# Optimization experiments

Hardware: AMD Instinct MI355X
Metric: run time of the kernel (lower is better)

Reference implementation:

```python
import jax, jax.numpy as jnp
import numpy as np

HIDDEN = 2048
N_HEADS = 32
N_KV_HEADS = 8
HEAD_DIM = HIDDEN // N_HEADS  # 64
N_GROUPS = N_HEADS // N_KV_HEADS  # 4
B, S = 1, 2048
NEG_INF = -1e9


def setup_inputs() -> dict:
    key = jax.random.key(0)
    k1, k2, k3, k4, k5 = jax.random.split(key, 5)
    hidden_states = jax.random.normal(k1, (B, S, HIDDEN), dtype=jnp.float32)
    # additive causal mask [B,1,S,S]
    causal = jnp.triu(jnp.full((S, S), NEG_INF, dtype=jnp.float32), k=1)
    attention_mask = jnp.broadcast_to(causal[None, None], (B, 1, S, S))
    position_ids = jnp.broadcast_to(jnp.arange(S, dtype=jnp.int32)[None], (B, S))
    scale = 0.02
    Wq = jax.random.normal(k2, (HIDDEN, N_HEADS * HEAD_DIM), dtype=jnp.float32) * scale
    Wk = jax.random.normal(k3, (HIDDEN, N_KV_HEADS * HEAD_DIM), dtype=jnp.float32) * scale
    Wv = jax.random.normal(k4, (HIDDEN, N_KV_HEADS * HEAD_DIM), dtype=jnp.float32) * scale
    Wo = jax.random.normal(k5, (HIDDEN, HIDDEN), dtype=jnp.float32) * scale
    return {"hidden_states": hidden_states, "attention_mask": attention_mask,
            "position_ids": position_ids, "Wq": Wq, "Wk": Wk, "Wv": Wv, "Wo": Wo}


def _rotate_half(x):
    x1, x2 = jnp.split(x, 2, axis=-1)
    return jnp.concatenate([-x2, x1], axis=-1)


def _rope_tables(kv_seq_len):
    inv_freq = 1.0 / (10000.0 ** (jnp.arange(0, HEAD_DIM, 2, dtype=jnp.float32) / HEAD_DIM))
    pos = jnp.arange(kv_seq_len, dtype=jnp.float32)
    freqs = pos[:, None] * inv_freq[None, :]          # [S, HD/2]
    emb = jnp.concatenate([freqs, freqs], axis=-1)    # [S, HD]
    return jnp.sin(emb), jnp.cos(emb)


def reference(hidden_states, attention_mask, position_ids, Wq, Wk, Wv, Wo):
    b, s, _ = hidden_states.shape
    q = (hidden_states @ Wq).reshape(b, s, N_HEADS, HEAD_DIM).transpose(0, 2, 1, 3)
    k = (hidden_states @ Wk).reshape(b, s, N_KV_HEADS, HEAD_DIM).transpose(0, 2, 1, 3)
    v = (hidden_states @ Wv).reshape(b, s, N_KV_HEADS, HEAD_DIM).transpose(0, 2, 1, 3)

    sin, cos = _rope_tables(s)
    cos_p = cos[position_ids][:, None]  # [B,1,S,HD]
    sin_p = sin[position_ids][:, None]
    q = q * cos_p + _rotate_half(q) * sin_p
    k = k * cos_p + _rotate_half(k) * sin_p

    # GQA: repeat_interleave kv heads along head axis
    k = jnp.repeat(k, N_GROUPS, axis=1)  # [B,H,S,HD]
    v = jnp.repeat(v, N_GROUPS, axis=1)

    q = q / jnp.sqrt(jnp.asarray(HEAD_DIM, q.dtype))
    scores = jnp.einsum('bhqd,bhkd->bhqk', q, k) + attention_mask
    attn = jax.nn.softmax(scores, axis=-1)
    out = jnp.einsum('bhqk,bhkd->bhqd', attn, v)
    out = out.transpose(0, 2, 1, 3).reshape(b, s, HIDDEN)
    return out @ Wo
```

## Files before the change

kernel.cpp:

```cpp
#include <hip/hip_runtime.h>
#include <hip/hip_bf16.h>

#define S_LEN 2048
#define HID 2048

typedef __attribute__((ext_vector_type(8))) short s16x8;
typedef __attribute__((ext_vector_type(4))) float f32x4;
typedef unsigned short u16;

__device__ __forceinline__ u16 f2bf(float f) {
  __hip_bfloat16 h = __float2bfloat16(f);
  return __builtin_bit_cast(u16, h);
}
__device__ __forceinline__ float bf2f(u16 u) {
  __hip_bfloat16 h = __builtin_bit_cast(__hip_bfloat16, u);
  return __bfloat162float(h);
}

#define GLD16(dst, src)                                                        \
  __builtin_amdgcn_global_load_lds(                                            \
      (__attribute__((address_space(1))) void*)(src),                          \
      (__attribute__((address_space(3))) void*)(dst), 16, 0, 0)

__global__ __launch_bounds__(256) void f2b_kernel(const float* __restrict__ in,
                                                  u16* __restrict__ outp, int n4) {
  int idx = blockIdx.x * 256 + threadIdx.x;
  if (idx >= n4) return;
  float4 v = *((const float4*)in + idx);
  ushort4 o;
  o.x = f2bf(v.x); o.y = f2bf(v.y); o.z = f2bf(v.z); o.w = f2bf(v.w);
  *((ushort4*)outp + idx) = o;
}

__global__ __launch_bounds__(256) void wtrans_kernel(const float* __restrict__ in,
                                                     u16* __restrict__ outp, int K, int N) {
  __shared__ u16 tile[32][33];
  int n0 = blockIdx.x * 32, k0 = blockIdx.y * 32;
  int tx = threadIdx.x & 31, ty = threadIdx.x >> 5;
#pragma unroll
  for (int r = 0; r < 4; ++r) {
    int row = ty + r * 8;
    tile[row][tx] = f2bf(in[(size_t)(k0 + row) * N + n0 + tx]);
  }
  __syncthreads();
#pragma unroll
  for (int r = 0; r < 4; ++r) {
    int row = ty + r * 8;
    outp[(size_t)(n0 + row) * K + k0 + tx] = tile[tx][row];
  }
}

__global__ __launch_bounds__(256) void wtransQKV_kernel(const float* __restrict__ Wq,
                                                        const float* __restrict__ Wk,
                                                        const float* __restrict__ Wv,
                                                        u16* __restrict__ outp) {
  __shared__ u16 tile[32][33];
  int n0g = blockIdx.x * 32, k0 = blockIdx.y * 32;
  const float* src;
  int n0, N;
  if (n0g < 2048)      { src = Wq; n0 = n0g;        N = 2048; }
  else if (n0g < 2560) { src = Wk; n0 = n0g - 2048; N = 512; }
  else                 { src = Wv; n0 = n0g - 2560; N = 512; }
  int tx = threadIdx.x & 31, ty = threadIdx.x >> 5;
#pragma unroll
  for (int r = 0; r < 4; ++r) {
    int row = ty + r * 8;
    tile[row][tx] = f2bf(src[(size_t)(k0 + row) * N + n0 + tx]);
  }
  __syncthreads();
#pragma unroll
  for (int r = 0; r < 4; ++r) {
    int row = ty + r * 8;
    outp[(size_t)(n0g + row) * HID + k0 + tx] = tile[tx][row];
  }
}

template <bool OUT_F32>
__global__ __launch_bounds__(256) void gemm_bt_kernel(const u16* __restrict__ A,
                                                      const u16* __restrict__ Bt,
                                                      void* __restrict__ C,
                                                      int N, int K, int sx) {
  __shared__ u16 lA[2][64 * 64];
  __shared__ u16 lB[2][128 * 64];
  int tid = threadIdx.x;
  int lane = tid & 63, w = tid >> 6;
  int lo = lane & 15, hi = lane >> 4;
  int wr = w >> 1, wc = w & 1;
  int blk = blockIdx.x;
  int j = blk & 7, q = blk >> 3;
  int bx = j * sx + (q % sx);
  int by = q / sx;
  int brow = by * 64, bcol = bx * 128;
  int l8 = lane >> 3;
  int cs = ((lane & 7) ^ l8) * 8;

  f32x4 z = {0.f, 0.f, 0.f, 0.f};
  f32x4 acc[2][4];
#pragma unroll
  for (int m = 0; m < 2; ++m)
#pragma unroll
    for (int n = 0; n < 4; ++n) acc[m][n] = z;

  const u16* Abase = A + (size_t)brow * K;
  const u16* Bbase = Bt + (size_t)bcol * K;

#define GSTAGE(buf, k0)                                                                   \
  {                                                                                       \
    _Pragma("unroll") for (int r2 = 0; r2 < 2; ++r2) {                                    \
      int c = r2 * 4 + w;                                                                 \
      GLD16(&lA[buf][c * 512], Abase + (size_t)(c * 8 + l8) * K + (k0) + cs);             \
    }                                                                                     \
    _Pragma("unroll") for (int r2 = 0; r2 < 4; ++r2) {                                    \
      int c = r2 * 4 + w;                                                                 \
      GLD16(&lB[buf][c * 512], Bbase + (size_t)(c * 8 + l8) * K + (k0) + cs);             \
    }                                                                                     \
  }

  int nsteps = K >> 6;
  int cur = 0;
  GSTAGE(0, 0);
  __syncthreads();

  for (int t = 0; t < nsteps; ++t) {
    if (t + 1 < nsteps) GSTAGE(cur ^ 1, (t + 1) * 64);

    s16x8 af[2][2], bfr[4][2];
#pragma unroll
    for (int m = 0; m < 2; ++m)
#pragma unroll
      for (int kk = 0; kk < 2; ++kk)
        af[m][kk] = *(const s16x8*)(&lA[cur][0] + (size_t)(wr * 32 + m * 16 + lo) * 64 +
                                    ((kk * 4 + hi) ^ (lo & 7)) * 8);
#pragma unroll
    for (int n = 0; n < 4; ++n)
#pragma unroll
      for (int kk = 0; kk < 2; ++kk)
        bfr[n][kk] = *(const s16x8*)(&lB[cur][0] + (size_t)(wc * 64 + n * 16 + lo) * 64 +
                                     ((kk * 4 + hi) ^ (lo & 7)) * 8);
    __builtin_amdgcn_s_setprio(1);
#pragma unroll
    for (int kk = 0; kk < 2; ++kk)
#pragma unroll
      for (int m = 0; m < 2; ++m)
#pragma unroll
        for (int n = 0; n < 4; ++n)
          acc[m][n] = __builtin_amdgcn_mfma_f32_16x16x32_bf16(af[m][kk], bfr[n][kk], acc[m][n], 0, 0, 0);
    __builtin_amdgcn_s_setprio(0);
    __syncthreads();
    cur ^= 1;
  }
#undef GSTAGE

#pragma unroll
  for (int m = 0; m < 2; ++m)
#pragma unroll
    for (int n = 0; n < 4; ++n)
#pragma unroll
      for (int r = 0; r < 4; ++r) {
        int row = brow + wr * 32 + m * 16 + hi * 4 + r;
        int col = bcol + wc * 64 + n * 16 + lo;
        if (OUT_F32)
          ((float*)C)[(size_t)row * N + col] = acc[m][n][r];
        else
          ((u16*)C)[(size_t)row * N + col] = f2bf(acc[m][n][r]);
      }
}

__global__ __launch_bounds__(256) void rope_kernel(const u16* __restrict__ in,
                                                   u16* __restrict__ Qout,
                                                   u16* __restrict__ Kout,
                                                   const int* __restrict__ pos_ids) {
  int idx = blockIdx.x * 256 + threadIdx.x;
  int i = idx & 31;
  int t2 = idx >> 5;
  int hh, s;
  const u16* base;
  u16* outp;
  float scale;
  if (t2 < S_LEN * 32) {
    hh = t2 & 31; s = t2 >> 5;
    base = in + (size_t)s * 3072 + hh * 64;
    outp = Qout + ((size_t)hh * S_LEN + s) * 64;
    scale = 0.125f * 1.44269504f;
  } else {
    int t3 = t2 - S_LEN * 32;
    hh = t3 & 7; s = t3 >> 3;
    base = in + (size_t)s * 3072 + 2048 + hh * 64;
    outp = Kout + ((size_t)hh * S_LEN + s) * 64;
    scale = 1.0f;
  }
  float pos = (float)pos_ids[s];
  float inv = exp2f(-(float)i * (13.2877124f / 32.f));
  float ang = pos * inv;
  float c = cosf(ang), sn = sinf(ang);
  float q1 = bf2f(base[i]);
  float q2 = bf2f(base[i + 32]);
  outp[i] = f2bf((q1 * c - q2 * sn) * scale);
  outp[i + 32] = f2bf((q2 * c + q1 * sn) * scale);
}

__global__ __launch_bounds__(256) void vtrans_kernel(const u16* __restrict__ in,
                                                     u16* __restrict__ outp,
                                                     int in_stride, int in_off) {
  __shared__ u16 tile[32][33];
  int s0 = blockIdx.x * 32, d0 = blockIdx.y * 32;
  int tx = threadIdx.x & 31, ty = threadIdx.x >> 5;
#pragma unroll
  for (int r = 0; r < 4; ++r) {
    int row = ty + r * 8;
    tile[row][tx] = in[(size_t)(s0 + row) * in_stride + in_off + d0 + tx];
  }
  __syncthreads();
#pragma unroll
  for (int r = 0; r < 4; ++r) {
    int row = ty + r * 8;
    outp[(size_t)(d0 + row) * S_LEN + s0 + tx] = tile[tx][row];
  }
}

__global__ __launch_bounds__(512) void attn_kernel(const u16* __restrict__ Qr,
                                                   const u16* __restrict__ Kr,
                                                   const u16* __restrict__ Vt,
                                                   u16* __restrict__ AO) {
  __shared__ u16 lK[2][2][64 * 64];
  __shared__ u16 lV[2][2][64 * 64];
  __shared__ u16 lP[8][16 * 64];
  int g = blockIdx.x & 7;
  int qt = 63 - (blockIdx.x >> 3);
  int q0 = qt * 32;
  int tid = threadIdx.x, lane = tid & 63, w = tid >> 6;
  int lo = lane & 15, hi = lane >> 4;
  int w2 = w >> 2;
  int h = g * 4 + (w & 3);
  int tmax = (q0 + 31) >> 7;
  int l8 = lane >> 3;
  int cs = ((lane & 7) ^ l8) * 8;

  const u16* Kbase = Kr + (size_t)g * S_LEN * 64;
  const u16* Vbase = Vt + (size_t)g * 64 * S_LEN;
  u16* Pw = &lP[w][0];

#define STAGE_KV(buf, t)                                                                  \
  {                                                                                       \
    _Pragma("unroll") for (int hs = 0; hs < 2; ++hs) {                                    \
      GLD16(&lK[buf][hs][w * 512],                                                        \
            Kbase + ((size_t)((t) * 128 + hs * 64 + w * 8 + l8)) * 64 + cs);              \
      GLD16(&lV[buf][hs][w * 512],                                                        \
            Vbase + ((size_t)(w * 8 + l8)) * S_LEN + (t) * 128 + hs * 64 + cs);           \
    }                                                                                     \
  }

  f32x4 z = {0.f, 0.f, 0.f, 0.f};

  s16x8 aq[2];
  {
    const u16* qp = Qr + ((size_t)h * S_LEN + q0 + w2 * 16) * 64;
#pragma unroll
    for (int kk = 0; kk < 2; ++kk)
      aq[kk] = *(const s16x8*)(qp + (size_t)lo * 64 + kk * 32 + hi * 8);
  }

  f32x4 oacc[4];
#pragma unroll
  for (int n = 0; n < 4; ++n) oacc[n] = z;
  float mrun[4], ps[4];
#pragma unroll
  for (int r = 0; r < 4; ++r) { mrun[r] = -1e30f; ps[r] = 0.f; }

  int cur = 0;
  STAGE_KV(0, 0);
  __syncthreads();

  for (int t = 0; t <= tmax; ++t) {
    if (t < tmax) STAGE_KV(cur ^ 1, t + 1);

    f32x4 sacc[2][4];
#pragma unroll
    for (int hs = 0; hs < 2; ++hs)
#pragma unroll
      for (int n = 0; n < 4; ++n) sacc[hs][n] = z;
    __builtin_amdgcn_s_setprio(1);
#pragma unroll
    for (int hs = 0; hs < 2; ++hs)
#pragma unroll
      for (int kk = 0; kk < 2; ++kk)
#pragma unroll
        for (int n = 0; n < 4; ++n) {
          s16x8 bk = *(const s16x8*)(&lK[cur][hs][0] + (size_t)(n * 16 + lo) * 64 +
                                     ((kk * 4 + hi) ^ (lo & 7)) * 8);
          sacc[hs][n] = __builtin_amdgcn_mfma_f32_16x16x32_bf16(aq[kk], bk, sacc[hs][n], 0, 0, 0);
        }
    __builtin_amdgcn_s_setprio(0);

    if (t == tmax) {
#pragma unroll
      for (int hs = 0; hs < 2; ++hs)
#pragma unroll
        for (int n = 0; n < 4; ++n)
#pragma unroll
          for (int r = 0; r < 4; ++r) {
            int qg = q0 + w2 * 16 + hi * 4 + r;
            int kg = t * 128 + hs * 64 + n * 16 + lo;
            if (kg > qg) sacc[hs][n][r] = -1e30f;
          }
    }

    float tm[4];
#pragma unroll
    for (int r = 0; r < 4; ++r) {
      float a = fmaxf(fmaxf(sacc[0][0][r], sacc[0][1][r]), fmaxf(sacc[0][2][r], sacc[0][3][r]));
      float b = fmaxf(fmaxf(sacc[1][0][r], sacc[1][1][r]), fmaxf(sacc[1][2][r], sacc[1][3][r]));
      tm[r] = fmaxf(a, b);
    }
#pragma unroll
    for (int off = 1; off < 16; off <<= 1)
#pragma unroll
      for (int r = 0; r < 4; ++r) tm[r] = fmaxf(tm[r], __shfl_xor(tm[r], off, 64));

    float growth = -1e30f;
#pragma unroll
    for (int r = 0; r < 4; ++r) growth = fmaxf(growth, tm[r] - mrun[r]);
    if (__any(growth > 12.f)) {
#pragma unroll
      for (int r = 0; r < 4; ++r) {
        float nm = fmaxf(mrun[r], tm[r]);
        float scl = __builtin_amdgcn_exp2f(mrun[r] - nm);
        mrun[r] = nm;
        ps[r] *= scl;
#pragma unroll
        for (int n = 0; n < 4; ++n) oacc[n][r] *= scl;
      }
    }
#pragma unroll
    for (int hs = 0; hs < 2; ++hs)
#pragma unroll
      for (int n = 0; n < 4; ++n)
#pragma unroll
        for (int r = 0; r < 4; ++r)
          sacc[hs][n][r] = __builtin_amdgcn_exp2f(sacc[hs][n][r] - mrun[r]);
#pragma unroll
    for (int r = 0; r < 4; ++r)
      ps[r] += sacc[0][0][r] + sacc[0][1][r] + sacc[0][2][r] + sacc[0][3][r] +
               sacc[1][0][r] + sacc[1][1][r] + sacc[1][2][r] + sacc[1][3][r];

#pragma unroll
    for (int hs = 0; hs < 2; ++hs) {
#pragma unroll
      for (int r = 0; r < 4; ++r) {
        int row = hi * 4 + r;
#pragma unroll
        for (int n = 0; n < 4; ++n) {
          int col = (n * 16 + lo) ^ ((row & 7) * 8);
          Pw[row * 64 + col] = f2bf(sacc[hs][n][r]);
        }
      }
      __builtin_amdgcn_s_setprio(1);
#pragma unroll
      for (int kk = 0; kk < 2; ++kk) {
        s16x8 ap = *(const s16x8*)(Pw + (size_t)lo * 64 + ((kk * 4 + hi) ^ (lo & 7)) * 8);
#pragma unroll
        for (int n = 0; n < 4; ++n) {
          s16x8 bv = *(const s16x8*)(&lV[cur][hs][0] + (size_t)(n * 16 + lo) * 64 +
                                     ((kk * 4 + hi) ^ (lo & 7)) * 8);
          oacc[n] = __builtin_amdgcn_mfma_f32_16x16x32_bf16(ap, bv, oacc[n], 0, 0, 0);
        }
      }
      __builtin_amdgcn_s_setprio(0);
    }

    __syncthreads();
    cur ^= 1;
  }

#pragma unroll
  for (int off = 1; off < 16; off <<= 1)
#pragma unroll
    for (int r = 0; r < 4; ++r) ps[r] += __shfl_xor(ps[r], off, 64);

#pragma unroll
  for (int n = 0; n < 4; ++n)
#pragma unroll
    for (int r = 0; r < 4; ++r) {
      int q = q0 + w2 * 16 + hi * 4 + r;
      int d = n * 16 + lo;
      AO[(size_t)q * HID + h * 64 + d] = f2bf(oacc[n][r] / ps[r]);
    }
#undef STAGE_KV
}

extern "C" void kernel_launch(void* const* d_in, const int* in_sizes, int n_in,
                              void* d_out, int out_size, void* d_ws, size_t ws_size,
                              hipStream_t stream) {
  const float* X  = (const float*)d_in[0];
  const int*   pos = (const int*)d_in[2];
  const float* Wq = (const float*)d_in[3];
  const float* Wk = (const float*)d_in[4];
  const float* Wv = (const float*)d_in[5];
  const float* Wo = (const float*)d_in[6];
  float* out = (float*)d_out;

  u16* Xb    = (u16*)d_ws;
  u16* WQKVt = Xb + (size_t)HID * HID;
  u16* Kr    = WQKVt;
  u16* Vt    = WQKVt + (size_t)8 * S_LEN * 64;
  u16* Wot   = WQKVt + (size_t)16 * S_LEN * 64;
  u16* QKVp  = WQKVt + (size_t)3072 * HID;
  u16* Qr    = Xb;
  u16* AO    = QKVp;

  f2b_kernel<<<(S_LEN * HID / 4 + 255) / 256, 256, 0, stream>>>(X, Xb, S_LEN * HID / 4);
  wtransQKV_kernel<<<dim3(3072 / 32, HID / 32), 256, 0, stream>>>(Wq, Wk, Wv, WQKVt);

  gemm_bt_kernel<false><<<dim3(768), 256, 0, stream>>>(Xb, WQKVt, QKVp, 3072, HID, 3);

  wtrans_kernel<<<dim3(HID / 32, HID / 32), 256, 0, stream>>>(Wo, Wot, HID, HID);

  rope_kernel<<<(S_LEN * 40 * 32) / 256, 256, 0, stream>>>(QKVp, Qr, Kr, pos);
  vtrans_kernel<<<dim3(S_LEN / 32, 512 / 32), 256, 0, stream>>>(QKVp, Vt, 3072, 2560);

  attn_kernel<<<dim3(512), 512, 0, stream>>>(Qr, Kr, Vt, AO);

  gemm_bt_kernel<true><<<dim3(512), 256, 0, stream>>>(AO, Wot, out, HID, HID, 2);
}
```

Before: 240.3 us.

## Enlarge GEMM tiles to 128x128 with 8 waves and vectorize weight transposes

The bf16 GEMM block tile grows from 64x128 with 4 waves to 128x128 with 8 waves, so each block reuses the staged B tile across twice as many rows and the grid shrinks by half. The weight transpose kernels switch to 64x64 tiles that read with float4 loads and write 16-byte vectors, aiming to cut memory transactions in the preprocessing stage. Trade-offs are more LDS per block, fewer blocks for the 256-CU device (the output GEMM drops to 256 blocks), and possible LDS bank conflicts on the column reads of the transpose tile.

```diff
diff --git a/kernel.cpp b/kernel.cpp
--- a/kernel.cpp
+++ b/kernel.cpp
@@ -32,74 +32,79 @@
   *((ushort4*)outp + idx) = o;
 }
 
-__global__ __launch_bounds__(256) void wtrans_kernel(const float* __restrict__ in,
-                                                     u16* __restrict__ outp, int K, int N) {
-  __shared__ u16 tile[32][33];
-  int n0 = blockIdx.x * 32, k0 = blockIdx.y * 32;
-  int tx = threadIdx.x & 31, ty = threadIdx.x >> 5;
-#pragma unroll
-  for (int r = 0; r < 4; ++r) {
-    int row = ty + r * 8;
-    tile[row][tx] = f2bf(in[(size_t)(k0 + row) * N + n0 + tx]);
+__device__ __forceinline__ void wtrans64_body(const float* __restrict__ src, int N,
+                                              u16* __restrict__ outp, int orow0,
+                                              int n0, int k0, int tid) {
+  __shared__ u16 tile[64][66];
+  int tr = tid >> 4;
+  int tc4 = (tid & 15) * 4;
+#pragma unroll
+  for (int rr = 0; rr < 4; ++rr) {
+    int r = tr + rr * 16;
+    float4 v = *(const float4*)&src[(size_t)(k0 + r) * N + n0 + tc4];
+    tile[r][tc4 + 0] = f2bf(v.x);
+    tile[r][tc4 + 1] = f2bf(v.y);
+    tile[r][tc4 + 2] = f2bf(v.z);
+    tile[r][tc4 + 3] = f2bf(v.w);
   }
   __syncthreads();
-#pragma unroll
-  for (int r = 0; r < 4; ++r) {
-    int row = ty + r * 8;
-    outp[(size_t)(n0 + row) * K + k0 + tx] = tile[tx][row];
-  }
+  int n = tid >> 2;
+  int k16 = (tid & 3) * 16;
+  s16x8 a, b;
+#pragma unroll
+  for (int j = 0; j < 8; ++j) {
+    a[j] = (short)tile[k16 + j][n];
+    b[j] = (short)tile[k16 + 8 + j][n];
+  }
+  u16* dst = outp + (size_t)(orow0 + n) * HID + k0 + k16;
+  *(s16x8*)dst = a;
+  *(s16x8*)(dst + 8) = b;
 }
 
 __global__ __launch_bounds__(256) void wtransQKV_kernel(const float* __restrict__ Wq,
                                                         const float* __restrict__ Wk,
                                                         const float* __restrict__ Wv,
                                                         u16* __restrict__ outp) {
-  __shared__ u16 tile[32][33];
-  int n0g = blockIdx.x * 32, k0 = blockIdx.y * 32;
+  int n0g = blockIdx.x * 64, k0 = blockIdx.y * 64;
   const float* src;
   int n0, N;
   if (n0g < 2048)      { src = Wq; n0 = n0g;        N = 2048; }
   else if (n0g < 2560) { src = Wk; n0 = n0g - 2048; N = 512; }
   else                 { src = Wv; n0 = n0g - 2560; N = 512; }
-  int tx = threadIdx.x & 31, ty = threadIdx.x >> 5;
-#pragma unroll
-  for (int r = 0; r < 4; ++r) {
-    int row = ty + r * 8;
-    tile[row][tx] = f2bf(src[(size_t)(k0 + row) * N + n0 + tx]);
-  }
-  __syncthreads();
-#pragma unroll
-  for (int r = 0; r < 4; ++r) {
-    int row = ty + r * 8;
-    outp[(size_t)(n0g + row) * HID + k0 + tx] = tile[tx][row];
-  }
+  wtrans64_body(src, N, outp, n0g, n0, k0, threadIdx.x);
+}
+
+__global__ __launch_bounds__(256) void wtransO_kernel(const float* __restrict__ Wo,
+                                                      u16* __restrict__ outp) {
+  int n0 = blockIdx.x * 64, k0 = blockIdx.y * 64;
+  wtrans64_body(Wo, 2048, outp, n0, n0, k0, threadIdx.x);
 }
 
 template <bool OUT_F32>
-__global__ __launch_bounds__(256) void gemm_bt_kernel(const u16* __restrict__ A,
-                                                      const u16* __restrict__ Bt,
-                                                      void* __restrict__ C,
-                                                      int N, int K, int sx) {
-  __shared__ u16 lA[2][64 * 64];
+__global__ __launch_bounds__(512, 4) void gemm_bt_kernel(const u16* __restrict__ A,
+                                                         const u16* __restrict__ Bt,
+                                                         void* __restrict__ C,
+                                                         int N, int K, int sx) {
+  __shared__ u16 lA[2][128 * 64];
   __shared__ u16 lB[2][128 * 64];
   int tid = threadIdx.x;
   int lane = tid & 63, w = tid >> 6;
   int lo = lane & 15, hi = lane >> 4;
-  int wr = w >> 1, wc = w & 1;
+  int wr = w >> 2, wc = w & 3;
   int blk = blockIdx.x;
   int j = blk & 7, q = blk >> 3;
   int bx = j * sx + (q % sx);
   int by = q / sx;
-  int brow = by * 64, bcol = bx * 128;
+  int brow = by * 128, bcol = bx * 128;
   int l8 = lane >> 3;
   int cs = ((lane & 7) ^ l8) * 8;
 
   f32x4 z = {0.f, 0.f, 0.f, 0.f};
-  f32x4 acc[2][4];
-#pragma unroll
-  for (int m = 0; m < 2; ++m)
-#pragma unroll
-    for (int n = 0; n < 4; ++n) acc[m][n] = z;
+  f32x4 acc[4][2];
+#pragma unroll
+  for (int m = 0; m < 4; ++m)
+#pragma unroll
+    for (int n = 0; n < 2; ++n) acc[m][n] = z;
 
   const u16* Abase = A + (size_t)brow * K;
   const u16* Bbase = Bt + (size_t)bcol * K;
@@ -107,11 +112,8 @@
 #define GSTAGE(buf, k0)                                                                   \
   {                                                                                       \
     _Pragma("unroll") for (int r2 = 0; r2 < 2; ++r2) {                                    \
-      int c = r2 * 4 + w;                                                                 \
+      int c = r2 * 8 + w;                                                                 \
       GLD16(&lA[buf][c * 512], Abase + (size_t)(c * 8 + l8) * K + (k0) + cs);             \
-    }                                                                                     \
-    _Pragma("unroll") for (int r2 = 0; r2 < 4; ++r2) {                                    \
-      int c = r2 * 4 + w;                                                                 \
       GLD16(&lB[buf][c * 512], Bbase + (size_t)(c * 8 + l8) * K + (k0) + cs);             \
     }                                                                                     \
   }
@@ -124,26 +126,26 @@
   for (int t = 0; t < nsteps; ++t) {
     if (t + 1 < nsteps) GSTAGE(cur ^ 1, (t + 1) * 64);
 
-    s16x8 af[2][2], bfr[4][2];
-#pragma unroll
-    for (int m = 0; m < 2; ++m)
+    s16x8 af[4][2], bfr[2][2];
+#pragma unroll
+    for (int m = 0; m < 4; ++m)
 #pragma unroll
       for (int kk = 0; kk < 2; ++kk)
-        af[m][kk] = *(const s16x8*)(&lA[cur][0] + (size_t)(wr * 32 + m * 16 + lo) * 64 +
+        af[m][kk] = *(const s16x8*)(&lA[cur][0] + (size_t)(wr * 64 + m * 16 + lo) * 64 +
                                     ((kk * 4 + hi) ^ (lo & 7)) * 8);
 #pragma unroll
-    for (int n = 0; n < 4; ++n)
+    for (int n = 0; n < 2; ++n)
 #pragma unroll
       for (int kk = 0; kk < 2; ++kk)
-        bfr[n][kk] = *(const s16x8*)(&lB[cur][0] + (size_t)(wc * 64 + n * 16 + lo) * 64 +
+        bfr[n][kk] = *(const s16x8*)(&lB[cur][0] + (size_t)(wc * 32 + n * 16 + lo) * 64 +
                                      ((kk * 4 + hi) ^ (lo & 7)) * 8);
     __builtin_amdgcn_s_setprio(1);
 #pragma unroll
     for (int kk = 0; kk < 2; ++kk)
 #pragma unroll
-      for (int m = 0; m < 2; ++m)
-#pragma unroll
-        for (int n = 0; n < 4; ++n)
+      for (int m = 0; m < 4; ++m)
+#pragma unroll
+        for (int n = 0; n < 2; ++n)
           acc[m][n] = __builtin_amdgcn_mfma_f32_16x16x32_bf16(af[m][kk], bfr[n][kk], acc[m][n], 0, 0, 0);
     __builtin_amdgcn_s_setprio(0);
     __syncthreads();
@@ -152,13 +154,13 @@
 #undef GSTAGE
 
 #pragma unroll
-  for (int m = 0; m < 2; ++m)
-#pragma unroll
-    for (int n = 0; n < 4; ++n)
+  for (int m = 0; m < 4; ++m)
+#pragma unroll
+    for (int n = 0; n < 2; ++n)
 #pragma unroll
       for (int r = 0; r < 4; ++r) {
-        int row = brow + wr * 32 + m * 16 + hi * 4 + r;
-        int col = bcol + wc * 64 + n * 16 + lo;
+        int row = brow + wr * 64 + m * 16 + hi * 4 + r;
+        int col = bcol + wc * 32 + n * 16 + lo;
         if (OUT_F32)
           ((float*)C)[(size_t)row * N + col] = acc[m][n][r];
         else
@@ -409,16 +411,16 @@
   u16* AO    = QKVp;
 
   f2b_kernel<<<(S_LEN * HID / 4 + 255) / 256, 256, 0, stream>>>(X, Xb, S_LEN * HID / 4);
-  wtransQKV_kernel<<<dim3(3072 / 32, HID / 32), 256, 0, stream>>>(Wq, Wk, Wv, WQKVt);
-
-  gemm_bt_kernel<false><<<dim3(768), 256, 0, stream>>>(Xb, WQKVt, QKVp, 3072, HID, 3);
-
-  wtrans_kernel<<<dim3(HID / 32, HID / 32), 256, 0, stream>>>(Wo, Wot, HID, HID);
+  wtransQKV_kernel<<<dim3(3072 / 64, HID / 64), 256, 0, stream>>>(Wq, Wk, Wv, WQKVt);
+
+  gemm_bt_kernel<false><<<dim3(384), 512, 0, stream>>>(Xb, WQKVt, QKVp, 3072, HID, 3);
+
+  wtransO_kernel<<<dim3(HID / 64, HID / 64), 256, 0, stream>>>(Wo, Wot);
 
   rope_kernel<<<(S_LEN * 40 * 32) / 256, 256, 0, stream>>>(QKVp, Qr, Kr, pos);
   vtrans_kernel<<<dim3(S_LEN / 32, 512 / 32), 256, 0, stream>>>(QKVp, Vt, 3072, 2560);
 
   attn_kernel<<<dim3(512), 512, 0, stream>>>(Qr, Kr, Vt, AO);
 
-  gemm_bt_kernel<true><<<dim3(512), 256, 0, stream>>>(AO, Wot, out, HID, HID, 2);
-}
+  gemm_bt_kernel<true><<<dim3(256), 512, 0, stream>>>(AO, Wot, out, HID, HID, 2);
+}
```

Result: no change. 244.0 us (+1.5%).
